# Kernel optimization log

Hardware: AMD Instinct MI355X
Metric: run time of the kernel (lower is better)

## Reference

```python
import jax, jax.numpy as jnp
import numpy as np
from jax import lax

NFRAMES = 8
LAM = 0.1
SEQLEN, BS, DF = 25, 256, 16384  # 5-way 5-shot support, 256 queries, ResNet-50 feats per frame


def l2norm(x, eps=1e-12):
    return x / jnp.maximum(jnp.linalg.norm(x, axis=-1, keepdims=True), eps)


def dp(D, lam=LAM):
    """OTAM-style soft alignment DP.
    D: [B, n, n] frame cosine-similarity matrices.
    Returns [B] soft-max alignment scores (lam * logsumexp relaxation).
    Matches the torch code: DP[:,:,0]=D[:,:,0]; row 0 is a cumulative sum;
    DP[:,1:,i] = lam*logsumexp([DP[:,:-1,i-1], DP[:,1:,i-1]]/lam) + D[:,1:,i];
    result = lam*logsumexp(DP[:,:,-1]/lam).
    """
    col0 = D[:, :, 0]                       # [B, n]
    cols = jnp.moveaxis(D[:, :, 1:], 2, 0)  # [n-1, B, n] columns i=1..n-1

    def step(prev, d_col):
        # prev: DP column i-1, [B, n]; d_col: D column i, [B, n]
        two = jnp.stack([prev[:, :-1], prev[:, 1:]], axis=-1)      # [B, n-1, 2]
        lse = lam * jax.nn.logsumexp(two / lam, axis=-1)           # [B, n-1]
        row0 = prev[:, :1] + d_col[:, :1]                          # cumsum on row 0
        new = jnp.concatenate([row0, lse + d_col[:, 1:]], axis=1)  # [B, n]
        return new, None

    last, _ = lax.scan(step, col0, cols)    # last column of DP, [B, n]
    return lam * jax.nn.logsumexp(last / lam, axis=-1)             # [B]


def setup_inputs() -> dict:
    key = jax.random.key(0)
    k1, k2 = jax.random.split(key)
    support_vecs = jax.random.normal(k1, (SEQLEN, BS, DF), dtype=jnp.float32)
    target_vec = jax.random.normal(k2, (BS, DF), dtype=jnp.float32)
    return {"support_vecs": support_vecs, "target_vec": target_vec}


def reference(support_vecs, target_vec):
    seqlen, bs, df = support_vecs.shape
    n = NFRAMES
    sv = l2norm(support_vecs.reshape(seqlen, bs, n, -1))   # [S, B, n, f]
    tv = l2norm(target_vec.reshape(bs, n, -1))             # [B, n, f]
    # D[s,b,i,j] = <sv[s,b,i], tv[b,j]> : [S, B, n, n]
    D = jnp.einsum('sbif,bjf->sbij', sv, tv)
    Dflat = D.reshape(seqlen * bs, n, n)
    sim = 0.5 * (dp(Dflat) + dp(jnp.swapaxes(Dflat, 1, 2)))
    return sim.reshape(seqlen, bs)
```

## Files before the change

### kernel.cpp

```cpp
#include <hip/hip_runtime.h>
#include <hip/hip_bf16.h>


constexpr int kNF   = 8;
constexpr int kFLEN = 2048;
constexpr int kSeq  = 25;
constexpr int kBS   = 256;
constexpr int kDF   = 16384;
constexpr float kLam    = 0.1f;
constexpr float kInvLam = 10.0f;

__global__ __launch_bounds__(256, 2) void otam_kernel(
    const float* __restrict__ sv,
    const float* __restrict__ tv,
    float* __restrict__ out)
{
    __shared__ float V[kDF];
    __shared__ float sdot[kNF][kNF];
    __shared__ float snu[kNF];
    __shared__ float snv[kNF];
    __shared__ float sD[kNF][kNF];

    const int bid = blockIdx.x;
    const int s = bid % kSeq;
    const int b = bid / kSeq;
    const int t = threadIdx.x;

    {
        const float4* tv4 = (const float4*)(tv + (size_t)b * kDF);
        float4* V4 = (float4*)V;
        #pragma unroll
        for (int it = 0; it < 16; ++it)
            V4[it * 256 + t] = tv4[it * 256 + t];
    }
    __syncthreads();

    const int g = t >> 5;
    const int l = t & 31;

    float v2 = 0.f;
    {
        const float4* Vg = (const float4*)(V + g * kFLEN);
        #pragma unroll 4
        for (int c = 0; c < 16; ++c) {
            float4 v = Vg[c * 32 + l];
            v2 = fmaf(v.x, v.x, v2); v2 = fmaf(v.y, v.y, v2);
            v2 = fmaf(v.z, v.z, v2); v2 = fmaf(v.w, v.w, v2);
        }
    }

    float dot[kNF] = {};
    float u2 = 0.f;
    const float4* U4 = (const float4*)(sv + ((size_t)s * kBS + b) * kDF + (size_t)g * kFLEN);
    #pragma unroll 4
    for (int c = 0; c < 16; ++c) {
        float4 u = U4[c * 32 + l];
        u2 = fmaf(u.x, u.x, fmaf(u.y, u.y, fmaf(u.z, u.z, fmaf(u.w, u.w, u2))));
        #pragma unroll
        for (int j = 0; j < kNF; ++j) {
            float4 v = ((const float4*)(V + j * kFLEN))[c * 32 + l];
            dot[j] = fmaf(u.x, v.x, fmaf(u.y, v.y, fmaf(u.z, v.z, fmaf(u.w, v.w, dot[j]))));
        }
    }

    #pragma unroll
    for (int m = 16; m >= 1; m >>= 1) {
        u2 += __shfl_xor(u2, m, 64);
        v2 += __shfl_xor(v2, m, 64);
        #pragma unroll
        for (int j = 0; j < kNF; ++j) dot[j] += __shfl_xor(dot[j], m, 64);
    }
    if (l == 0) {
        snu[g] = u2;
        snv[g] = v2;
        #pragma unroll
        for (int j = 0; j < kNF; ++j) sdot[g][j] = dot[j];
    }
    __syncthreads();

    if (t < 64) {
        const int i = t >> 3, j = t & 7;
        sD[i][j] = sdot[i][j] * rsqrtf(snu[i]) * rsqrtf(snv[j]);
    }
    __syncthreads();

    if (t < 16) {
        const int r = t & 7;
        const bool xp = (t >= 8);

        auto Dm = [&](int rr, int ii) -> float {
            return xp ? sD[ii][rr] : sD[rr][ii];
        };

        float prev = Dm(r, 0);
        #pragma unroll
        for (int i = 1; i < kNF; ++i) {
            float up = __shfl_up(prev, 1, 64);
            float d  = Dm(r, i);
            float mx = fmaxf(up, prev);
            float mn = fminf(up, prev);
            float lse = mx + kLam * log1pf(expf((mn - mx) * kInvLam));
            prev = (r == 0) ? (prev + d) : (lse + d);
        }
        float mx = prev;
        #pragma unroll
        for (int m = 4; m >= 1; m >>= 1) mx = fmaxf(mx, __shfl_xor(mx, m, 64));
        float e = expf((prev - mx) * kInvLam);
        #pragma unroll
        for (int m = 4; m >= 1; m >>= 1) e += __shfl_xor(e, m, 64);
        float res = mx + kLam * logf(e);

        float resT = __shfl(res, (t & 7) + 8, 64);
        if (t == 0) out[(size_t)s * kBS + b] = 0.5f * (res + resT);
    }
}

extern "C" void kernel_launch(void* const* d_in, const int* in_sizes, int n_in,
                              void* d_out, int out_size, void* d_ws, size_t ws_size,
                              hipStream_t stream) {
    const float* sv = (const float*)d_in[0];
    const float* tv = (const float*)d_in[1];
    float* out = (float*)d_out;
    otam_kernel<<<dim3(kSeq * kBS), dim3(256), 0, stream>>>(sv, tv, out);
}
```

Measured before the change: 573.4 us.

## Use one wavefront per (s,b) pair with register-tiled 8x8 dots and no LDS

Replaces the 256-thread block that staged the target vector in shared memory with a single 64-lane wavefront per output element. Each lane loads all 8 support and 8 target float4 slices per chunk and accumulates the full 8x8 dot and norm matrix in registers, then reduces it with cross-lane shuffles. The DP runs redundantly in every lane with fast exp/log intrinsics, so shared memory and block barriers are gone. The costs are heavy register pressure from 64 accumulators plus 16 float4 loads, a long shuffle reduction of 80 values, and the block index mapping changed so consecutive blocks share the same s instead of the same b.

```diff
diff --git a/kernel.cpp b/kernel.cpp
--- a/kernel.cpp
+++ b/kernel.cpp
@@ -3,116 +3,105 @@
 
 
 constexpr int kNF   = 8;
-constexpr int kFLEN = 2048;
 constexpr int kSeq  = 25;
 constexpr int kBS   = 256;
 constexpr int kDF   = 16384;
 constexpr float kLam    = 0.1f;
 constexpr float kInvLam = 10.0f;
 
-__global__ __launch_bounds__(256, 2) void otam_kernel(
+__global__ __launch_bounds__(64, 2) void otam_kernel(
     const float* __restrict__ sv,
     const float* __restrict__ tv,
     float* __restrict__ out)
 {
-    __shared__ float V[kDF];
-    __shared__ float sdot[kNF][kNF];
-    __shared__ float snu[kNF];
-    __shared__ float snv[kNF];
-    __shared__ float sD[kNF][kNF];
+    const int bid = blockIdx.x;
+    const int b = bid % kBS;
+    const int s = bid / kBS;
+    const int l = threadIdx.x;
 
-    const int bid = blockIdx.x;
-    const int s = bid % kSeq;
-    const int b = bid / kSeq;
-    const int t = threadIdx.x;
+    const float4* __restrict__ U = (const float4*)(sv + ((size_t)s * kBS + b) * kDF);
+    const float4* __restrict__ V = (const float4*)(tv + (size_t)b * kDF);
 
-    {
-        const float4* tv4 = (const float4*)(tv + (size_t)b * kDF);
-        float4* V4 = (float4*)V;
+    float acc[kNF][kNF] = {};
+    float un[kNF] = {};
+    float vn[kNF] = {};
+
+    #pragma unroll 2
+    for (int c = 0; c < 8; ++c) {
+        float4 vv[kNF], uu[kNF];
         #pragma unroll
-        for (int it = 0; it < 16; ++it)
-            V4[it * 256 + t] = tv4[it * 256 + t];
-    }
-    __syncthreads();
+        for (int j = 0; j < kNF; ++j) vv[j] = V[j * 512 + c * 64 + l];
+        #pragma unroll
+        for (int i = 0; i < kNF; ++i) uu[i] = U[i * 512 + c * 64 + l];
 
-    const int g = t >> 5;
-    const int l = t & 31;
-
-    float v2 = 0.f;
-    {
-        const float4* Vg = (const float4*)(V + g * kFLEN);
-        #pragma unroll 4
-        for (int c = 0; c < 16; ++c) {
-            float4 v = Vg[c * 32 + l];
-            v2 = fmaf(v.x, v.x, v2); v2 = fmaf(v.y, v.y, v2);
-            v2 = fmaf(v.z, v.z, v2); v2 = fmaf(v.w, v.w, v2);
-        }
-    }
-
-    float dot[kNF] = {};
-    float u2 = 0.f;
-    const float4* U4 = (const float4*)(sv + ((size_t)s * kBS + b) * kDF + (size_t)g * kFLEN);
-    #pragma unroll 4
-    for (int c = 0; c < 16; ++c) {
-        float4 u = U4[c * 32 + l];
-        u2 = fmaf(u.x, u.x, fmaf(u.y, u.y, fmaf(u.z, u.z, fmaf(u.w, u.w, u2))));
         #pragma unroll
-        for (int j = 0; j < kNF; ++j) {
-            float4 v = ((const float4*)(V + j * kFLEN))[c * 32 + l];
-            dot[j] = fmaf(u.x, v.x, fmaf(u.y, v.y, fmaf(u.z, v.z, fmaf(u.w, v.w, dot[j]))));
-        }
+        for (int i = 0; i < kNF; ++i)
+            un[i] = fmaf(uu[i].x, uu[i].x, fmaf(uu[i].y, uu[i].y,
+                    fmaf(uu[i].z, uu[i].z, fmaf(uu[i].w, uu[i].w, un[i]))));
+        #pragma unroll
+        for (int j = 0; j < kNF; ++j)
+            vn[j] = fmaf(vv[j].x, vv[j].x, fmaf(vv[j].y, vv[j].y,
+                    fmaf(vv[j].z, vv[j].z, fmaf(vv[j].w, vv[j].w, vn[j]))));
+        #pragma unroll
+        for (int i = 0; i < kNF; ++i)
+            #pragma unroll
+            for (int j = 0; j < kNF; ++j)
+                acc[i][j] = fmaf(uu[i].x, vv[j].x, fmaf(uu[i].y, vv[j].y,
+                            fmaf(uu[i].z, vv[j].z, fmaf(uu[i].w, vv[j].w, acc[i][j]))));
     }
 
     #pragma unroll
-    for (int m = 16; m >= 1; m >>= 1) {
-        u2 += __shfl_xor(u2, m, 64);
-        v2 += __shfl_xor(v2, m, 64);
+    for (int m = 32; m >= 1; m >>= 1) {
         #pragma unroll
-        for (int j = 0; j < kNF; ++j) dot[j] += __shfl_xor(dot[j], m, 64);
+        for (int i = 0; i < kNF; ++i) {
+            un[i] += __shfl_xor(un[i], m, 64);
+            vn[i] += __shfl_xor(vn[i], m, 64);
+        }
+        #pragma unroll
+        for (int i = 0; i < kNF; ++i)
+            #pragma unroll
+            for (int j = 0; j < kNF; ++j)
+                acc[i][j] += __shfl_xor(acc[i][j], m, 64);
     }
-    if (l == 0) {
-        snu[g] = u2;
-        snv[g] = v2;
+
+    float ru[kNF], rv[kNF];
+    #pragma unroll
+    for (int i = 0; i < kNF; ++i) { ru[i] = rsqrtf(un[i]); rv[i] = rsqrtf(vn[i]); }
+    float D[kNF][kNF];
+    #pragma unroll
+    for (int i = 0; i < kNF; ++i)
         #pragma unroll
-        for (int j = 0; j < kNF; ++j) sdot[g][j] = dot[j];
-    }
-    __syncthreads();
+        for (int j = 0; j < kNF; ++j)
+            D[i][j] = acc[i][j] * ru[i] * rv[j];
 
-    if (t < 64) {
-        const int i = t >> 3, j = t & 7;
-        sD[i][j] = sdot[i][j] * rsqrtf(snu[i]) * rsqrtf(snv[j]);
-    }
-    __syncthreads();
+    auto lse2 = [](float a, float bb) {
+        float mx = fmaxf(a, bb), mn = fminf(a, bb);
+        return mx + kLam * __logf(1.f + __expf((mn - mx) * kInvLam));
+    };
 
-    if (t < 16) {
-        const int r = t & 7;
-        const bool xp = (t >= 8);
-
-        auto Dm = [&](int rr, int ii) -> float {
-            return xp ? sD[ii][rr] : sD[rr][ii];
-        };
-
-        float prev = Dm(r, 0);
+    float res[2];
+    #pragma unroll
+    for (int t = 0; t < 2; ++t) {
+        float prev[kNF];
+        #pragma unroll
+        for (int r = 0; r < kNF; ++r) prev[r] = t ? D[0][r] : D[r][0];
         #pragma unroll
         for (int i = 1; i < kNF; ++i) {
-            float up = __shfl_up(prev, 1, 64);
-            float d  = Dm(r, i);
-            float mx = fmaxf(up, prev);
-            float mn = fminf(up, prev);
-            float lse = mx + kLam * log1pf(expf((mn - mx) * kInvLam));
-            prev = (r == 0) ? (prev + d) : (lse + d);
+            #pragma unroll
+            for (int r = kNF - 1; r >= 1; --r)
+                prev[r] = lse2(prev[r - 1], prev[r]) + (t ? D[i][r] : D[r][i]);
+            prev[0] += (t ? D[i][0] : D[0][i]);
         }
-        float mx = prev;
+        float mx = prev[0];
         #pragma unroll
-        for (int m = 4; m >= 1; m >>= 1) mx = fmaxf(mx, __shfl_xor(mx, m, 64));
-        float e = expf((prev - mx) * kInvLam);
+        for (int r = 1; r < kNF; ++r) mx = fmaxf(mx, prev[r]);
+        float e = 0.f;
         #pragma unroll
-        for (int m = 4; m >= 1; m >>= 1) e += __shfl_xor(e, m, 64);
-        float res = mx + kLam * logf(e);
+        for (int r = 0; r < kNF; ++r) e += __expf((prev[r] - mx) * kInvLam);
+        res[t] = mx + kLam * __logf(e);
+    }
 
-        float resT = __shfl(res, (t & 7) + 8, 64);
-        if (t == 0) out[(size_t)s * kBS + b] = 0.5f * (res + resT);
-    }
+    if (l == 0) out[(size_t)s * kBS + b] = 0.5f * (res[0] + res[1]);
 }
 
 extern "C" void kernel_launch(void* const* d_in, const int* in_sizes, int n_in,
@@ -121,5 +110,5 @@
     const float* sv = (const float*)d_in[0];
     const float* tv = (const float*)d_in[1];
     float* out = (float*)d_out;
-    otam_kernel<<<dim3(kSeq * kBS), dim3(256), 0, stream>>>(sv, tv, out);
+    otam_kernel<<<dim3(kSeq * kBS), dim3(64), 0, stream>>>(sv, tv, out);
 }
```

Result: slower. 614.0 us (+7.1%).
